# Performance work log

Measured on AMD Instinct MI355X. Metric: run time of the kernel, lower is better.

The kernel has to match this reference:

```python
import jax, jax.numpy as jnp
import numpy as np

NUM_WIRES = 18
NUM_LAYERS = 3
BATCH = 64
DIM = 2 ** NUM_WIRES


def _apply_ry(psi, theta, w):
    # RY(t) = [[cos(t/2), -sin(t/2)], [sin(t/2), cos(t/2)]] on wire w (wire 0 = MSB)
    B = psi.shape[0]
    c = jnp.cos(theta * 0.5).astype(psi.dtype)
    s = jnp.sin(theta * 0.5).astype(psi.dtype)
    p = psi.reshape(B, 2 ** w, 2, -1)
    a, b = p[:, :, 0], p[:, :, 1]
    return jnp.stack([c * a - s * b, s * a + c * b], axis=2).reshape(B, -1)


def _apply_rz(psi, theta, w):
    # RZ(t) = diag(e^{-i t/2}, e^{+i t/2}) on wire w
    B = psi.shape[0]
    half = (theta * 0.5).astype(jnp.complex64)
    p0 = jnp.exp(-1j * half)
    p1 = jnp.exp(1j * half)
    p = psi.reshape(B, 2 ** w, 2, -1)
    return jnp.stack([p0 * p[:, :, 0], p1 * p[:, :, 1]], axis=2).reshape(B, -1)


def _apply_cnot_adjacent(psi, w):
    # CNOT with control w, target w+1: flip target bit where control bit = 1
    B = psi.shape[0]
    p = psi.reshape(B, 2 ** w, 2, 2, -1)
    p = p.at[:, :, 1].set(p[:, :, 1, ::-1])
    return p.reshape(B, -1)


def _expval_z(psi, w):
    # <Z_w> = P(bit_w = 0) - P(bit_w = 1)
    B = psi.shape[0]
    prob = (psi.real ** 2 + psi.imag ** 2).reshape(B, 2 ** w, 2, -1)
    p = prob.sum(axis=(1, 3))  # (B, 2)
    return p[:, 0] - p[:, 1]


def _circuit(psi, params):
    for layer in range(params.shape[0]):
        for w in range(NUM_WIRES):
            psi = _apply_ry(psi, params[layer, 0, w], w)
            psi = _apply_rz(psi, params[layer, 1, w], w)
        for w in range(NUM_WIRES - 1):
            psi = _apply_cnot_adjacent(psi, w)
    # expvals of PauliZ on every wire -> (B, num_wires)
    return jnp.stack([_expval_z(psi, w) for w in range(NUM_WIRES)], axis=-1)


def setup_inputs() -> dict:
    key = jax.random.key(0)
    k1, k2, k3, k4, k5 = jax.random.split(key, 5)
    state_re = jax.random.normal(k1, (BATCH, DIM), dtype=jnp.float32)
    state_im = jax.random.normal(k2, (BATCH, DIM), dtype=jnp.float32)
    norm = jnp.sqrt(jnp.sum(state_re ** 2 + state_im ** 2, axis=-1, keepdims=True))
    state_re = state_re / norm
    state_im = state_im / norm
    params = jax.random.normal(k3, (NUM_LAYERS, 2, NUM_WIRES), dtype=jnp.float32)
    head_w = jax.random.normal(k4, (1, NUM_WIRES), dtype=jnp.float32) / np.sqrt(NUM_WIRES)
    head_b = jax.random.normal(k5, (1,), dtype=jnp.float32) / np.sqrt(NUM_WIRES)
    return {"state_re": state_re, "state_im": state_im, "params": params,
            "head_w": head_w, "head_b": head_b}


def reference(state_re, state_im, params, head_w, head_b):
    psi = (state_re + 1j * state_im).astype(jnp.complex64)  # (B, 2^n)
    feats = _circuit(psi, params)                            # (B, n)
    out = feats @ head_w.T + head_b                          # (B, 1)
    return out[:, 0]
```

## Files before the change

### kernel.cpp

```cpp
#include <hip/hip_runtime.h>


static __device__ __forceinline__ int phys(int m) {
    return m + 4 * ((m >> 6) + (m >> 9));
}

template<int J>
__device__ __forceinline__ void sqg(float* ar, float* ai, float c, float s, float pc, float ps) {
#pragma unroll
    for (int r = 0; r < 32; ++r) {
        if (((r >> J) & 1) == 0) {
            const int r1 = r + (1 << J);
            const float a0r = ar[r], a0i = ai[r], a1r = ar[r1], a1i = ai[r1];
            ar[r] = fmaf(c, a0r, -(s * a1r));
            ai[r] = fmaf(c, a0i, -(s * a1i));
            const float t1r = fmaf(s, a0r, c * a1r);
            const float t1i = fmaf(s, a0i, c * a1i);
            ar[r1] = fmaf(pc, t1r, -(ps * t1i));
            ai[r1] = fmaf(pc, t1i,  (ps * t1r));
        }
    }
}

template<int JC, int JT>
__device__ __forceinline__ void cnotg(float* ar, float* ai) {
#pragma unroll
    for (int r = 0; r < 32; ++r) {
        if (((r >> JC) & 1) == 1 && ((r >> JT) & 1) == 0) {
            const int r1 = r + (1 << JT);
            float tr = ar[r]; ar[r] = ar[r1]; ar[r1] = tr;
            float ti = ai[r]; ai[r] = ai[r1]; ai[r1] = ti;
        }
    }
}

__global__ __launch_bounds__(128) void passB_k(float* __restrict__ re, float* __restrict__ im,
                                               const float* __restrict__ params, int layer)
{
    __shared__ float lre[4384], lim[4384];
    const int t    = threadIdx.x;
    const int b    = blockIdx.x >> 6;
    const int mid  = blockIdx.x & 63;
    const int base = (b << 18) | (mid << 5);

    float C[7], S[7], PC[7], PS[7];
    const float* pl = params + layer * 36;
#pragma unroll
    for (int k = 0; k < 7; ++k) {
        const int w = 6 - k;
        __sincosf(0.5f * pl[w], &S[k], &C[k]);
        __sincosf(pl[18 + w], &PS[k], &PC[k]);
    }

    float ar[32], ai[32];
#pragma unroll
    for (int r = 0; r < 32; ++r) {
        const int n = base + (r << 13) + ((t >> 5) << 11) + (t & 31);
        ar[r] = re[n]; ai[r] = im[n];
    }
    sqg<4>(ar, ai, C[6], S[6], PC[6], PS[6]);
    sqg<3>(ar, ai, C[5], S[5], PC[5], PS[5]);
    sqg<2>(ar, ai, C[4], S[4], PC[4], PS[4]);
    sqg<1>(ar, ai, C[3], S[3], PC[3], PS[3]);
    sqg<0>(ar, ai, C[2], S[2], PC[2], PS[2]);
    cnotg<4,3>(ar, ai);
    cnotg<3,2>(ar, ai);
    cnotg<2,1>(ar, ai);
    cnotg<1,0>(ar, ai);

#pragma unroll
    for (int r = 0; r < 32; ++r) {
        const int m = (r << 7) | t;
        lre[phys(m)] = ar[r]; lim[phys(m)] = ai[r];
    }
    __syncthreads();
#pragma unroll
    for (int g = 0; g < 8; ++g) {
        const int m = ((t >> 3) << 8) | (g << 5) | ((t & 7) << 2);
        const float4 vr = *(const float4*)&lre[phys(m)];
        const float4 vi = *(const float4*)&lim[phys(m)];
        ar[4*g+0] = vr.x; ar[4*g+1] = vr.y; ar[4*g+2] = vr.z; ar[4*g+3] = vr.w;
        ai[4*g+0] = vi.x; ai[4*g+1] = vi.y; ai[4*g+2] = vi.z; ai[4*g+3] = vi.w;
    }
    sqg<3>(ar, ai, C[1], S[1], PC[1], PS[1]);
    sqg<2>(ar, ai, C[0], S[0], PC[0], PS[0]);
    cnotg<4,3>(ar, ai);
    cnotg<3,2>(ar, ai);

#pragma unroll
    for (int g = 0; g < 8; ++g) {
        const int n = base + ((t >> 3) << 14) + (g << 11) + ((t & 7) << 2);
        *(float4*)&re[n] = make_float4(ar[4*g+0], ar[4*g+1], ar[4*g+2], ar[4*g+3]);
        *(float4*)&im[n] = make_float4(ai[4*g+0], ai[4*g+1], ai[4*g+2], ai[4*g+3]);
    }
}

template<bool FINAL>
__global__ __launch_bounds__(128) void passA_k(float* __restrict__ re, float* __restrict__ im,
                                               const float* __restrict__ params, int layer,
                                               const float* __restrict__ hw,
                                               const float* __restrict__ hb,
                                               float* __restrict__ out)
{
    __shared__ float lre[4384], lim[4384];
    const int t    = threadIdx.x;
    const int b    = blockIdx.x >> 6;
    const int hi   = blockIdx.x & 63;
    const int base = (b << 18) | (hi << 12);

    float C[11], S[11], PC[11], PS[11];
    const float* pl = params + layer * 36;
#pragma unroll
    for (int p = 0; p < 11; ++p) {
        const int w = 17 - p;
        __sincosf(0.5f * pl[w], &S[p], &C[p]);
        __sincosf(pl[18 + w], &PS[p], &PC[p]);
    }

    float ar[32], ai[32];
#pragma unroll
    for (int r = 0; r < 32; ++r) {
        const int n = base + (r << 7) + t;
        ar[r] = re[n]; ai[r] = im[n];
    }
    sqg<3>(ar, ai, C[10], S[10], PC[10], PS[10]);
    sqg<2>(ar, ai, C[9],  S[9],  PC[9],  PS[9]);
    sqg<1>(ar, ai, C[8],  S[8],  PC[8],  PS[8]);
    sqg<0>(ar, ai, C[7],  S[7],  PC[7],  PS[7]);
    cnotg<4,3>(ar, ai); cnotg<3,2>(ar, ai); cnotg<2,1>(ar, ai); cnotg<1,0>(ar, ai);

#pragma unroll
    for (int r = 0; r < 32; ++r) {
        const int m = (r << 7) | t;
        lre[phys(m)] = ar[r]; lim[phys(m)] = ai[r];
    }
    __syncthreads();
#pragma unroll
    for (int r = 0; r < 32; ++r) {
        const int m = ((t >> 3) << 8) | (r << 3) | (t & 7);
        ar[r] = lre[phys(m)]; ai[r] = lim[phys(m)];
    }
    sqg<3>(ar, ai, C[6], S[6], PC[6], PS[6]);
    sqg<2>(ar, ai, C[5], S[5], PC[5], PS[5]);
    sqg<1>(ar, ai, C[4], S[4], PC[4], PS[4]);
    sqg<0>(ar, ai, C[3], S[3], PC[3], PS[3]);
    cnotg<4,3>(ar, ai); cnotg<3,2>(ar, ai); cnotg<2,1>(ar, ai); cnotg<1,0>(ar, ai);

    __syncthreads();
#pragma unroll
    for (int r = 0; r < 32; ++r) {
        const int m = ((t >> 3) << 8) | (r << 3) | (t & 7);
        lre[phys(m)] = ar[r]; lim[phys(m)] = ai[r];
    }
    __syncthreads();
#pragma unroll
    for (int g = 0; g < 8; ++g) {
        const int m = (t << 5) | (g << 2);
        const float4 vr = *(const float4*)&lre[phys(m)];
        const float4 vi = *(const float4*)&lim[phys(m)];
        ar[4*g+0] = vr.x; ar[4*g+1] = vr.y; ar[4*g+2] = vr.z; ar[4*g+3] = vr.w;
        ai[4*g+0] = vi.x; ai[4*g+1] = vi.y; ai[4*g+2] = vi.z; ai[4*g+3] = vi.w;
    }
    sqg<2>(ar, ai, C[2], S[2], PC[2], PS[2]);
    sqg<1>(ar, ai, C[1], S[1], PC[1], PS[1]);
    sqg<0>(ar, ai, C[0], S[0], PC[0], PS[0]);
    cnotg<3,2>(ar, ai); cnotg<2,1>(ar, ai); cnotg<1,0>(ar, ai);

    if (!FINAL) {
        __syncthreads();
#pragma unroll
        for (int g = 0; g < 8; ++g) {
            const int m = (t << 5) | (g << 2);
            *(float4*)&lre[phys(m)] = make_float4(ar[4*g+0], ar[4*g+1], ar[4*g+2], ar[4*g+3]);
            *(float4*)&lim[phys(m)] = make_float4(ai[4*g+0], ai[4*g+1], ai[4*g+2], ai[4*g+3]);
        }
        __syncthreads();
#pragma unroll
        for (int g = 0; g < 8; ++g) {
            const int m = (g << 9) | (t << 2);
            const float4 vr = *(const float4*)&lre[phys(m)];
            const float4 vi = *(const float4*)&lim[phys(m)];
            const int n = base + (g << 9) + (t << 2);
            *(float4*)&re[n] = vr;
            *(float4*)&im[n] = vi;
        }
    } else {
        float accP = 0.f, D0 = 0.f, D1 = 0.f, D2 = 0.f, D3 = 0.f, D4 = 0.f;
#pragma unroll
        for (int r = 0; r < 32; ++r) {
            const float p = ar[r] * ar[r] + ai[r] * ai[r];
            accP += p;
            if (r & 1)  D0 -= p; else D0 += p;
            if (r & 2)  D1 -= p; else D1 += p;
            if (r & 4)  D2 -= p; else D2 += p;
            if (r & 8)  D3 -= p; else D3 += p;
            if (r & 16) D4 -= p; else D4 += p;
        }
        float G = 0.f;
#pragma unroll
        for (int k = 0; k < 7; ++k)
            G += ((t >> k) & 1) ? -hw[12 - k] : hw[12 - k];
#pragma unroll
        for (int k = 0; k < 6; ++k)
            G += ((hi >> k) & 1) ? -hw[5 - k] : hw[5 - k];
        float v = accP * G + D0 * hw[17] + D1 * hw[16] + D2 * hw[15] + D3 * hw[14] + D4 * hw[13];
        if (t == 0 && hi == 0) v += hb[0];
#pragma unroll
        for (int off = 32; off > 0; off >>= 1) v += __shfl_xor(v, off);
        if ((t & 63) == 0) atomicAdd(&out[b], v);
    }
}

extern "C" void kernel_launch(void* const* d_in, const int* in_sizes, int n_in,
                              void* d_out, int out_size, void* d_ws, size_t ws_size,
                              hipStream_t stream)
{
    float* re            = (float*)d_in[0];
    float* im            = (float*)d_in[1];
    const float* params  = (const float*)d_in[2];
    const float* hw      = (const float*)d_in[3];
    const float* hb      = (const float*)d_in[4];
    float* out           = (float*)d_out;
    (void)in_sizes; (void)n_in; (void)d_ws; (void)ws_size;

    hipMemsetAsync(out, 0, (size_t)out_size * sizeof(float), stream);

    const dim3 grid(4096), blk(128);
    for (int l = 0; l < 3; ++l) {
        passB_k<<<grid, blk, 0, stream>>>(re, im, params, l);
        if (l < 2) passA_k<false><<<grid, blk, 0, stream>>>(re, im, params, l, nullptr, nullptr, nullptr);
        else       passA_k<true ><<<grid, blk, 0, stream>>>(re, im, params, l, hw, hb, out);
    }
}
```

Baseline: 447.0 us.

## Collapse six passes into two kernels with bf16-packed intermediate state

Replaces the per-layer pair of kernels with two kernels. The first applies gates across all three layers for low wires using register/LDS transposes and permuted (folded CNOT) index mappings. It then writes the intermediate state as packed bf16 complex into the input buffer. The second kernel finishes the remaining gates and computes the weighted expectation directly. This cuts global memory traffic heavily but lowers the precision of the intermediate state to bf16, and it overwrites the input tensor in place.

```diff
diff --git a/kernel.cpp b/kernel.cpp
--- a/kernel.cpp
+++ b/kernel.cpp
@@ -1,234 +1,250 @@
 #include <hip/hip_runtime.h>
 
 
-static __device__ __forceinline__ int phys(int m) {
-    return m + 4 * ((m >> 6) + (m >> 9));
-}
-
+#define NW 36
+
+static __device__ __forceinline__ float rfl(float x){
+  return __int_as_float(__builtin_amdgcn_readfirstlane(__float_as_int(x)));
+}
+static __device__ __forceinline__ unsigned sfx11(unsigned x){
+  x ^= x>>1; x ^= x>>2; x ^= x>>4; x ^= x>>8; return x & 0x7FFu;
+}
+static __device__ __forceinline__ int lofs(int row, int pos){
+  return row*NW + (pos ^ (((row>>3)&7)<<2));
+}
+static __device__ __forceinline__ unsigned packbf(float a, float b){
+  unsigned ua = __float_as_uint(a); ua += 0x7FFFu + ((ua>>16)&1u);
+  unsigned ub = __float_as_uint(b); ub += 0x7FFFu + ((ub>>16)&1u);
+  return (ua>>16) | (ub & 0xFFFF0000u);
+}
+static __device__ __forceinline__ void unpack2(unsigned u, float& a, float& b){
+  a = __uint_as_float(u<<16); b = __uint_as_float(u & 0xFFFF0000u);
+}
+static __device__ __forceinline__ void sq_pair(float& a0r,float& a0i,float& a1r,float& a1i,
+                                               float c,float s,float pc,float ps){
+  const float t0r = fmaf(c,a0r,-(s*a1r));
+  const float t0i = fmaf(c,a0i,-(s*a1i));
+  const float t1r = fmaf(s,a0r, c*a1r);
+  const float t1i = fmaf(s,a0i, c*a1i);
+  a0r=t0r; a0i=t0i;
+  a1r = fmaf(pc,t1r,-(ps*t1i));
+  a1i = fmaf(pc,t1i, (ps*t1r));
+}
 template<int J>
-__device__ __forceinline__ void sqg(float* ar, float* ai, float c, float s, float pc, float ps) {
-#pragma unroll
-    for (int r = 0; r < 32; ++r) {
-        if (((r >> J) & 1) == 0) {
-            const int r1 = r + (1 << J);
-            const float a0r = ar[r], a0i = ai[r], a1r = ar[r1], a1i = ai[r1];
-            ar[r] = fmaf(c, a0r, -(s * a1r));
-            ai[r] = fmaf(c, a0i, -(s * a1i));
-            const float t1r = fmaf(s, a0r, c * a1r);
-            const float t1i = fmaf(s, a0i, c * a1i);
-            ar[r1] = fmaf(pc, t1r, -(ps * t1i));
-            ai[r1] = fmaf(pc, t1i,  (ps * t1r));
-        }
-    }
-}
-
-template<int JC, int JT>
-__device__ __forceinline__ void cnotg(float* ar, float* ai) {
-#pragma unroll
-    for (int r = 0; r < 32; ++r) {
-        if (((r >> JC) & 1) == 1 && ((r >> JT) & 1) == 0) {
-            const int r1 = r + (1 << JT);
-            float tr = ar[r]; ar[r] = ar[r1]; ar[r1] = tr;
-            float ti = ai[r]; ai[r] = ai[r1]; ai[r1] = ti;
-        }
-    }
-}
-
-__global__ __launch_bounds__(128) void passB_k(float* __restrict__ re, float* __restrict__ im,
-                                               const float* __restrict__ params, int layer)
+static __device__ __forceinline__ void sqg(float* ar,float* ai,float c,float s,float pc,float ps){
+#pragma unroll
+  for(int r=0;r<32;++r) if(((r>>J)&1)==0){
+    const int r1 = r + (1<<J);
+    sq_pair(ar[r],ai[r],ar[r1],ai[r1],c,s,pc,ps);
+  }
+}
+template<int J>
+static __device__ __forceinline__ void gate(float* ar,float* ai,const float* pl,int wire){
+  float sv,cv;
+  __sincosf(0.5f*pl[wire],&sv,&cv); const float s=rfl(sv), c=rfl(cv);
+  __sincosf(pl[18+wire],&sv,&cv);   const float ps=rfl(sv), pc=rfl(cv);
+  sqg<J>(ar,ai,c,s,pc,ps);
+}
+static __device__ __forceinline__ void gate_l5(float* ar,float* ai,const float* pl,int wire,int l){
+  float sv,cv;
+  __sincosf(0.5f*pl[wire],&sv,&cv); const float s=rfl(sv), c=rfl(cv);
+  __sincosf(pl[18+wire],&sv,&cv);   const float ps=rfl(sv), pc=rfl(cv);
+  const int side = (l>>5)&1;
+  const float bco = side ? s : -s;
+  const float qc  = side ? pc : 1.f;
+  const float qs  = side ? ps : 0.f;
+#pragma unroll
+  for(int r=0;r<32;++r){
+    const float pr = __shfl_xor(ar[r],32);
+    const float pi = __shfl_xor(ai[r],32);
+    const float tr = fmaf(c,ar[r],bco*pr);
+    const float ti = fmaf(c,ai[r],bco*pi);
+    ar[r] = fmaf(qc,tr,-(qs*ti));
+    ai[r] = fmaf(qc,ti, (qs*tr));
+  }
+}
+
+#define XPOSE(AEXPR)                                                          \
+  {                                                                           \
+    int a[32];                                                                \
+    _Pragma("unroll") for(int r=0;r<32;++r){ AEXPR; }                         \
+    _Pragma("unroll") for(int r=0;r<32;++r) Lb[a[r]] = ar[r];                 \
+    _Pragma("unroll") for(int q=0;q<8;++q){                                   \
+      const float4 v=*(const float4*)&Lb[lofs(l,q<<2)];                       \
+      ar[4*q]=v.x; ar[4*q+1]=v.y; ar[4*q+2]=v.z; ar[4*q+3]=v.w; }             \
+    _Pragma("unroll") for(int r=0;r<32;++r) Lb[a[r]] = ai[r];                 \
+    _Pragma("unroll") for(int q=0;q<8;++q){                                   \
+      const float4 v=*(const float4*)&Lb[lofs(l,q<<2)];                       \
+      ai[4*q]=v.x; ai[4*q+1]=v.y; ai[4*q+2]=v.z; ai[4*q+3]=v.w; }             \
+  }
+
+__global__ __launch_bounds__(256,4) void pass1_k(const float* re, const float* __restrict__ im,
+                                                 unsigned* up, const float* __restrict__ params)
 {
-    __shared__ float lre[4384], lim[4384];
-    const int t    = threadIdx.x;
-    const int b    = blockIdx.x >> 6;
-    const int mid  = blockIdx.x & 63;
-    const int base = (b << 18) | (mid << 5);
-
-    float C[7], S[7], PC[7], PS[7];
-    const float* pl = params + layer * 36;
-#pragma unroll
-    for (int k = 0; k < 7; ++k) {
-        const int w = 6 - k;
-        __sincosf(0.5f * pl[w], &S[k], &C[k]);
-        __sincosf(pl[18 + w], &PS[k], &PC[k]);
-    }
-
-    float ar[32], ai[32];
-#pragma unroll
-    for (int r = 0; r < 32; ++r) {
-        const int n = base + (r << 13) + ((t >> 5) << 11) + (t & 31);
-        ar[r] = re[n]; ai[r] = im[n];
-    }
-    sqg<4>(ar, ai, C[6], S[6], PC[6], PS[6]);
-    sqg<3>(ar, ai, C[5], S[5], PC[5], PS[5]);
-    sqg<2>(ar, ai, C[4], S[4], PC[4], PS[4]);
-    sqg<1>(ar, ai, C[3], S[3], PC[3], PS[3]);
-    sqg<0>(ar, ai, C[2], S[2], PC[2], PS[2]);
-    cnotg<4,3>(ar, ai);
-    cnotg<3,2>(ar, ai);
-    cnotg<2,1>(ar, ai);
-    cnotg<1,0>(ar, ai);
-
-#pragma unroll
-    for (int r = 0; r < 32; ++r) {
-        const int m = (r << 7) | t;
-        lre[phys(m)] = ar[r]; lim[phys(m)] = ai[r];
-    }
-    __syncthreads();
-#pragma unroll
-    for (int g = 0; g < 8; ++g) {
-        const int m = ((t >> 3) << 8) | (g << 5) | ((t & 7) << 2);
-        const float4 vr = *(const float4*)&lre[phys(m)];
-        const float4 vi = *(const float4*)&lim[phys(m)];
-        ar[4*g+0] = vr.x; ar[4*g+1] = vr.y; ar[4*g+2] = vr.z; ar[4*g+3] = vr.w;
-        ai[4*g+0] = vi.x; ai[4*g+1] = vi.y; ai[4*g+2] = vi.z; ai[4*g+3] = vi.w;
-    }
-    sqg<3>(ar, ai, C[1], S[1], PC[1], PS[1]);
-    sqg<2>(ar, ai, C[0], S[0], PC[0], PS[0]);
-    cnotg<4,3>(ar, ai);
-    cnotg<3,2>(ar, ai);
-
-#pragma unroll
-    for (int g = 0; g < 8; ++g) {
-        const int n = base + ((t >> 3) << 14) + (g << 11) + ((t & 7) << 2);
-        *(float4*)&re[n] = make_float4(ar[4*g+0], ar[4*g+1], ar[4*g+2], ar[4*g+3]);
-        *(float4*)&im[n] = make_float4(ai[4*g+0], ai[4*g+1], ai[4*g+2], ai[4*g+3]);
-    }
-}
-
-template<bool FINAL>
-__global__ __launch_bounds__(128) void passA_k(float* __restrict__ re, float* __restrict__ im,
-                                               const float* __restrict__ params, int layer,
-                                               const float* __restrict__ hw,
-                                               const float* __restrict__ hb,
-                                               float* __restrict__ out)
+  __shared__ __align__(16) float lds[4*2304];
+  const int t = threadIdx.x, l = t&63, j = t>>6;
+  float* Lb = lds + j*2304;
+  const int blk = blockIdx.x;
+  const int Xg = blk&7, q2 = blk>>3;
+  const int b = q2>>2, fq = (Xg<<2)|(q2&3);
+  const int f = (fq<<2)|j;
+  const unsigned base = ((unsigned)b<<18) | (unsigned)f;
+  const float* pl0 = params;
+  const float* pl1 = params+36;
+  const float* pl2 = params+72;
+
+  float ar[32], ai[32];
+#pragma unroll
+  for(int r=0;r<32;++r){
+    const unsigned n = base + (unsigned)(r<<13) + (unsigned)(l<<7);
+    ar[r]=re[n]; ai[r]=im[n];
+  }
+
+  gate<4>(ar,ai,pl0,0); gate<3>(ar,ai,pl0,1); gate<2>(ar,ai,pl0,2);
+  gate<1>(ar,ai,pl0,3); gate<0>(ar,ai,pl0,4);
+  XPOSE( a[r]=lofs((l&32)|r, l&31) )
+  gate<4>(ar,ai,pl0,6); gate<3>(ar,ai,pl0,7); gate<2>(ar,ai,pl0,8);
+  gate<1>(ar,ai,pl0,9); gate<0>(ar,ai,pl0,10);
+  gate_l5(ar,ai,pl0,5,l);
+  XPOSE( const unsigned w=((unsigned)(l&31)<<6)|((unsigned)(l>>5)<<5)|(unsigned)r; \
+         const unsigned wp=sfx11(w); a[r]=lofs((int)(wp&63u),(int)(wp>>6)) )
+
+  gate<4>(ar,ai,pl1,0); gate<3>(ar,ai,pl1,1); gate<2>(ar,ai,pl1,2);
+  gate<1>(ar,ai,pl1,3); gate<0>(ar,ai,pl1,4);
+  XPOSE( a[r]=lofs(((l&1)<<5)|r, l>>1) )
+  gate<4>(ar,ai,pl1,5); gate<3>(ar,ai,pl1,6); gate<2>(ar,ai,pl1,7);
+  gate<1>(ar,ai,pl1,8); gate<0>(ar,ai,pl1,9);
+  XPOSE( const unsigned w=((unsigned)(l&31)<<6)|((unsigned)r<<1)|(unsigned)(l>>5); \
+         const unsigned wp=(sfx11(w)&~1u)|(w&1u); a[r]=lofs((int)(wp&63u),(int)(wp>>6)) )
+
+  gate<4>(ar,ai,pl2,0); gate<3>(ar,ai,pl2,1); gate<2>(ar,ai,pl2,2);
+  gate<1>(ar,ai,pl2,3); gate<0>(ar,ai,pl2,4);
+  XPOSE( a[r]=lofs(((l&1)<<5)|r, l>>1) )
+  gate<4>(ar,ai,pl2,5); gate<3>(ar,ai,pl2,6); gate<2>(ar,ai,pl2,7);
+  gate<1>(ar,ai,pl2,8);
+#pragma unroll
+  for(int r=0;r<32;++r){
+    const unsigned w2 = ((unsigned)(l&31)<<6)|((unsigned)r<<1)|(unsigned)(l>>5);
+    const unsigned w3 = (sfx11(w2)&~3u)|(w2&3u);
+    const unsigned sg = ((w3>>4)<<11) | ((w3&15u)<<7) | (unsigned)f;
+    up[((unsigned)b<<18) | sg] = packbf(ar[r], ai[r]);
+  }
+}
+
+__global__ __launch_bounds__(128,4) void pass2_k(const unsigned* __restrict__ up,
+                                                 const float* __restrict__ params,
+                                                 const float* __restrict__ hw,
+                                                 const float* __restrict__ hb,
+                                                 float* __restrict__ out)
 {
-    __shared__ float lre[4384], lim[4384];
-    const int t    = threadIdx.x;
-    const int b    = blockIdx.x >> 6;
-    const int hi   = blockIdx.x & 63;
-    const int base = (b << 18) | (hi << 12);
-
-    float C[11], S[11], PC[11], PS[11];
-    const float* pl = params + layer * 36;
-#pragma unroll
-    for (int p = 0; p < 11; ++p) {
-        const int w = 17 - p;
-        __sincosf(0.5f * pl[w], &S[p], &C[p]);
-        __sincosf(pl[18 + w], &PS[p], &PC[p]);
-    }
-
-    float ar[32], ai[32];
-#pragma unroll
-    for (int r = 0; r < 32; ++r) {
-        const int n = base + (r << 7) + t;
-        ar[r] = re[n]; ai[r] = im[n];
-    }
-    sqg<3>(ar, ai, C[10], S[10], PC[10], PS[10]);
-    sqg<2>(ar, ai, C[9],  S[9],  PC[9],  PS[9]);
-    sqg<1>(ar, ai, C[8],  S[8],  PC[8],  PS[8]);
-    sqg<0>(ar, ai, C[7],  S[7],  PC[7],  PS[7]);
-    cnotg<4,3>(ar, ai); cnotg<3,2>(ar, ai); cnotg<2,1>(ar, ai); cnotg<1,0>(ar, ai);
-
-#pragma unroll
-    for (int r = 0; r < 32; ++r) {
-        const int m = (r << 7) | t;
-        lre[phys(m)] = ar[r]; lim[phys(m)] = ai[r];
-    }
-    __syncthreads();
-#pragma unroll
-    for (int r = 0; r < 32; ++r) {
-        const int m = ((t >> 3) << 8) | (r << 3) | (t & 7);
-        ar[r] = lre[phys(m)]; ai[r] = lim[phys(m)];
-    }
-    sqg<3>(ar, ai, C[6], S[6], PC[6], PS[6]);
-    sqg<2>(ar, ai, C[5], S[5], PC[5], PS[5]);
-    sqg<1>(ar, ai, C[4], S[4], PC[4], PS[4]);
-    sqg<0>(ar, ai, C[3], S[3], PC[3], PS[3]);
-    cnotg<4,3>(ar, ai); cnotg<3,2>(ar, ai); cnotg<2,1>(ar, ai); cnotg<1,0>(ar, ai);
-
-    __syncthreads();
-#pragma unroll
-    for (int r = 0; r < 32; ++r) {
-        const int m = ((t >> 3) << 8) | (r << 3) | (t & 7);
-        lre[phys(m)] = ar[r]; lim[phys(m)] = ai[r];
-    }
-    __syncthreads();
-#pragma unroll
-    for (int g = 0; g < 8; ++g) {
-        const int m = (t << 5) | (g << 2);
-        const float4 vr = *(const float4*)&lre[phys(m)];
-        const float4 vi = *(const float4*)&lim[phys(m)];
-        ar[4*g+0] = vr.x; ar[4*g+1] = vr.y; ar[4*g+2] = vr.z; ar[4*g+3] = vr.w;
-        ai[4*g+0] = vi.x; ai[4*g+1] = vi.y; ai[4*g+2] = vi.z; ai[4*g+3] = vi.w;
-    }
-    sqg<2>(ar, ai, C[2], S[2], PC[2], PS[2]);
-    sqg<1>(ar, ai, C[1], S[1], PC[1], PS[1]);
-    sqg<0>(ar, ai, C[0], S[0], PC[0], PS[0]);
-    cnotg<3,2>(ar, ai); cnotg<2,1>(ar, ai); cnotg<1,0>(ar, ai);
-
-    if (!FINAL) {
-        __syncthreads();
-#pragma unroll
-        for (int g = 0; g < 8; ++g) {
-            const int m = (t << 5) | (g << 2);
-            *(float4*)&lre[phys(m)] = make_float4(ar[4*g+0], ar[4*g+1], ar[4*g+2], ar[4*g+3]);
-            *(float4*)&lim[phys(m)] = make_float4(ai[4*g+0], ai[4*g+1], ai[4*g+2], ai[4*g+3]);
-        }
-        __syncthreads();
-#pragma unroll
-        for (int g = 0; g < 8; ++g) {
-            const int m = (g << 9) | (t << 2);
-            const float4 vr = *(const float4*)&lre[phys(m)];
-            const float4 vi = *(const float4*)&lim[phys(m)];
-            const int n = base + (g << 9) + (t << 2);
-            *(float4*)&re[n] = vr;
-            *(float4*)&im[n] = vi;
-        }
-    } else {
-        float accP = 0.f, D0 = 0.f, D1 = 0.f, D2 = 0.f, D3 = 0.f, D4 = 0.f;
-#pragma unroll
-        for (int r = 0; r < 32; ++r) {
-            const float p = ar[r] * ar[r] + ai[r] * ai[r];
-            accP += p;
-            if (r & 1)  D0 -= p; else D0 += p;
-            if (r & 2)  D1 -= p; else D1 += p;
-            if (r & 4)  D2 -= p; else D2 += p;
-            if (r & 8)  D3 -= p; else D3 += p;
-            if (r & 16) D4 -= p; else D4 += p;
-        }
-        float G = 0.f;
-#pragma unroll
-        for (int k = 0; k < 7; ++k)
-            G += ((t >> k) & 1) ? -hw[12 - k] : hw[12 - k];
-#pragma unroll
-        for (int k = 0; k < 6; ++k)
-            G += ((hi >> k) & 1) ? -hw[5 - k] : hw[5 - k];
-        float v = accP * G + D0 * hw[17] + D1 * hw[16] + D2 * hw[15] + D3 * hw[14] + D4 * hw[13];
-        if (t == 0 && hi == 0) v += hb[0];
-#pragma unroll
-        for (int off = 32; off > 0; off >>= 1) v += __shfl_xor(v, off);
-        if ((t & 63) == 0) atomicAdd(&out[b], v);
-    }
+  __shared__ __align__(16) float lds[2*2304];
+  const int t = threadIdx.x, l = t&63, wib = t>>6;
+  float* Lb = lds + wib*2304;
+  const int b = blockIdx.x>>6;
+  const int hi7 = ((blockIdx.x&63)<<1)|wib;
+  const unsigned base = ((unsigned)b<<18)|((unsigned)hi7<<11);
+  const float* pl0 = params;
+  const float* pl1 = params+36;
+  const float* pl2 = params+72;
+
+  uint4 U[8];
+#pragma unroll
+  for(int g=0; g<8; ++g)
+    U[g] = *(const uint4*)&up[base + (unsigned)(g<<8) + (unsigned)(l<<2)];
+
+  float c16,s16,pc16,ps16, c17,s17,pc17,ps17;
+  { float sv,cv;
+    __sincosf(0.5f*pl0[16],&sv,&cv); s16=rfl(sv); c16=rfl(cv);
+    __sincosf(pl0[18+16],&sv,&cv);   ps16=rfl(sv); pc16=rfl(cv);
+    __sincosf(0.5f*pl0[17],&sv,&cv); s17=rfl(sv); c17=rfl(cv);
+    __sincosf(pl0[18+17],&sv,&cv);   ps17=rfl(sv); pc17=rfl(cv); }
+
+  float ar[32], ai[32];
+#pragma unroll
+  for(int g=0; g<8; ++g){
+    unpack2(U[g].x, ar[4*g+0], ai[4*g+0]);
+    unpack2(U[g].y, ar[4*g+1], ai[4*g+1]);
+    unpack2(U[g].z, ar[4*g+2], ai[4*g+2]);
+    unpack2(U[g].w, ar[4*g+3], ai[4*g+3]);
+    sq_pair(ar[4*g+0],ai[4*g+0],ar[4*g+2],ai[4*g+2], c16,s16,pc16,ps16);
+    sq_pair(ar[4*g+1],ai[4*g+1],ar[4*g+3],ai[4*g+3], c16,s16,pc16,ps16);
+    sq_pair(ar[4*g+0],ai[4*g+0],ar[4*g+1],ai[4*g+1], c17,s17,pc17,ps17);
+    sq_pair(ar[4*g+2],ai[4*g+2],ar[4*g+3],ai[4*g+3], c17,s17,pc17,ps17);
+  }
+
+  XPOSE( a[r]=lofs(((r&0x1C)<<1)|((l>>5)<<2)|(r&3), l&31) )
+  gate<4>(ar,ai,pl0,11); gate<3>(ar,ai,pl0,12); gate<2>(ar,ai,pl0,13);
+  gate<1>(ar,ai,pl0,14); gate<0>(ar,ai,pl0,15);
+  XPOSE( const unsigned v=((unsigned)(l>>5)<<10)|((unsigned)((l>>4)&1)<<9)|((unsigned)((l>>3)&1)<<8) \
+              |((unsigned)((l>>2)&1)<<7)|((unsigned)r<<2)|((unsigned)((l>>1)&1)<<1)|(unsigned)(l&1);  \
+         const unsigned s=sfx11(v);                                                                    \
+         const unsigned vp=(v&0x780u)|((((s>>8)&1u)? (s^0x7Fu):s)&0x7Fu);                              \
+         a[r]=lofs((int)((((vp>>10)&1u)<<5)|(((vp>>9)&1u)<<4)|(((vp>>8)&1u)<<3)|(vp&7u)),              \
+                   (int)((vp>>3)&31u)) )
+  gate<4>(ar,ai,pl1,10); gate<3>(ar,ai,pl1,11); gate<2>(ar,ai,pl1,12);
+  gate<1>(ar,ai,pl1,13); gate<0>(ar,ai,pl1,14);
+  XPOSE( const unsigned v=((unsigned)(l>>5)<<10)|((unsigned)((l>>4)&1)<<9)|((unsigned)((l>>3)&1)<<8) \
+              |((unsigned)r<<3)|(unsigned)(l&7);                                                       \
+         a[r]=lofs((int)((v>>3)&63u), (int)(((v&7u)<<2)|(((v>>10)&1u)<<1)|((v>>9)&1u))) )
+  gate<4>(ar,ai,pl1,15); gate<3>(ar,ai,pl1,16); gate<2>(ar,ai,pl1,17);
+  XPOSE( const unsigned v=((unsigned)((r>>1)&1)<<10)|((unsigned)(r&1)<<9)|((unsigned)(l&63)<<3)       \
+              |((unsigned)((r>>4)&1)<<2)|((unsigned)((r>>3)&1)<<1)|(unsigned)((r>>2)&1);               \
+         const unsigned s=sfx11(v);                                                                    \
+         const unsigned vp=(v&0x700u)|((((s>>9)&1u)? (s^0xFFu):s)&0xFFu);                              \
+         a[r]=lofs((int)((((vp>>10)&1u)<<5)|(((vp>>9)&1u)<<4)|(vp&15u)), (int)((vp>>4)&31u)) )
+  gate<4>(ar,ai,pl2,9); gate<3>(ar,ai,pl2,10); gate<2>(ar,ai,pl2,11);
+  gate<1>(ar,ai,pl2,12); gate<0>(ar,ai,pl2,13);
+  XPOSE( const unsigned v=((unsigned)(l>>5)<<10)|((unsigned)((l>>4)&1)<<9)|((unsigned)r<<4)|(unsigned)(l&15); \
+         a[r]=lofs((int)((((v>>9)&1u)<<5)|((v>>4)&31u)), (int)(((v&15u)<<1)|((v>>10)&1u))) )
+  gate<4>(ar,ai,pl2,14); gate<3>(ar,ai,pl2,15); gate<2>(ar,ai,pl2,16);
+  gate<1>(ar,ai,pl2,17);
+
+  float Ghi = 0.f;
+#pragma unroll
+  for(int jj=0; jj<7; ++jj)
+    Ghi += ((hi7>>jj)&1) ? -hw[6-jj] : hw[6-jj];
+  const int pA = __popc(l&63)&1, p5 = __popc(l&62)&1, p6 = __popc(l&60)&1;
+  const int p7 = __popc(l&56)&1, p8 = __popc(l&48)&1, p9 = (l>>5)&1;
+  const float A0 = pA? -hw[17]:hw[17], A1 = pA? -hw[16]:hw[16];
+  const float A2 = pA? -hw[15]:hw[15], A3 = pA? -hw[14]:hw[14];
+  const float A4 = pA? -hw[13]:hw[13], A5 = p5? -hw[12]:hw[12];
+  const float A6 = p6? -hw[11]:hw[11], A7 = p7? -hw[10]:hw[10];
+  const float A8 = p8? -hw[9]:hw[9],  A9 = p9? -hw[8]:hw[8];
+  const float Hm = Ghi + A4 + A5 + A6 + A7 + A8 + A9;
+  const float h7 = hw[7];
+  float acc = 0.f;
+#pragma unroll
+  for(int r=0;r<32;++r){
+    const int e3 = (r>>4)&1;
+    const int e2 = e3 ^ ((r>>3)&1);
+    const int e1 = e2 ^ ((r>>2)&1);
+    const int e0 = e1 ^ ((r>>1)&1);
+    const int v10 = r&1;
+    const float W = Hm + (v10? -h7:h7) + (e3? -A3:A3) + (e2? -A2:A2)
+                       + (e1? -A1:A1) + (e0? -A0:A0);
+    acc = fmaf(fmaf(ar[r],ar[r], ai[r]*ai[r]), W, acc);
+  }
+  if (hi7==0 && l==0) acc += hb[0];
+#pragma unroll
+  for(int off=32; off>0; off>>=1) acc += __shfl_xor(acc, off);
+  if (l==0) atomicAdd(&out[b], acc);
 }
 
 extern "C" void kernel_launch(void* const* d_in, const int* in_sizes, int n_in,
                               void* d_out, int out_size, void* d_ws, size_t ws_size,
                               hipStream_t stream)
 {
-    float* re            = (float*)d_in[0];
-    float* im            = (float*)d_in[1];
-    const float* params  = (const float*)d_in[2];
-    const float* hw      = (const float*)d_in[3];
-    const float* hb      = (const float*)d_in[4];
-    float* out           = (float*)d_out;
-    (void)in_sizes; (void)n_in; (void)d_ws; (void)ws_size;
-
-    hipMemsetAsync(out, 0, (size_t)out_size * sizeof(float), stream);
-
-    const dim3 grid(4096), blk(128);
-    for (int l = 0; l < 3; ++l) {
-        passB_k<<<grid, blk, 0, stream>>>(re, im, params, l);
-        if (l < 2) passA_k<false><<<grid, blk, 0, stream>>>(re, im, params, l, nullptr, nullptr, nullptr);
-        else       passA_k<true ><<<grid, blk, 0, stream>>>(re, im, params, l, hw, hb, out);
-    }
-}
+  const float* re     = (const float*)d_in[0];
+  const float* im     = (const float*)d_in[1];
+  unsigned* up        = (unsigned*)d_in[0];
+  const float* params = (const float*)d_in[2];
+  const float* hw     = (const float*)d_in[3];
+  const float* hb     = (const float*)d_in[4];
+  float* out          = (float*)d_out;
+  (void)in_sizes; (void)n_in; (void)d_ws; (void)ws_size;
+
+  hipMemsetAsync(out, 0, (size_t)out_size * sizeof(float), stream);
+
+  pass1_k<<<dim3(2048), dim3(256), 0, stream>>>(re, im, up, params);
+  pass2_k<<<dim3(4096), dim3(128), 0, stream>>>(up, params, hw, hb, out);
+}
```

New measurement: 656.8 us. +46.9%, slower.
